# Kernel optimization log

Measured on AMD Instinct MI355X. Metric: run time of the kernel, lower is better.

## Reference

```python
import jax, jax.numpy as jnp
import numpy as np

N = 50000   # nodes
E = 1600000 # edges
G = 512     # graphs in batch
IN_DIM, EMBED, H, D = 64, 128, 4, 32
D1, D2, D3 = 128, 64, 16
NEG_SLOPE = 0.2  # DGL GATConv default


def setup_inputs() -> dict:
    key = jax.random.key(0)
    ks = jax.random.split(key, 16)
    def glorot(k, shape):
        fan = shape[0] + shape[-1]
        return jax.random.normal(k, shape, jnp.float32) * jnp.sqrt(2.0 / fan)
    return {
        "feature": jax.random.normal(ks[0], (N, IN_DIM), jnp.float32),
        "src": jax.random.randint(ks[1], (E,), 0, N, jnp.int32),
        "dst": jax.random.randint(ks[2], (E,), 0, N, jnp.int32),
        "graph_ids": jnp.sort(jax.random.randint(ks[3], (N,), 0, G, jnp.int32)),
        "W0": glorot(ks[4], (IN_DIM, EMBED)), "b0": jnp.zeros((EMBED,), jnp.float32),
        "Wfc": glorot(ks[5], (EMBED, H * D)),
        "attn_l": glorot(ks[6], (H, D)), "attn_r": glorot(ks[7], (H, D)),
        "gat_bias": jnp.zeros((H * D,), jnp.float32),
        "W1": glorot(ks[8], (H * D, D1)), "b1": jnp.zeros((D1,), jnp.float32),
        "W2": glorot(ks[9], (D1, D2)), "b2": jnp.zeros((D2,), jnp.float32),
        "W3": glorot(ks[10], (D2, D3)), "b3": jnp.zeros((D3,), jnp.float32),
    }


def reference(feature, src, dst, graph_ids, W0, b0, Wfc, attn_l, attn_r,
              gat_bias, W1, b1, W2, b2, W3, b3):
    # initial dense embed
    h = feature @ W0 + b0                                   # [N, EMBED]
    # GATConv
    feat = (h @ Wfc).reshape(N, H, D)                       # [N,H,D]
    el = jnp.einsum('nhd,hd->nh', feat, attn_l)             # [N,H]
    er = jnp.einsum('nhd,hd->nh', feat, attn_r)
    e = jax.nn.leaky_relu(el[src] + er[dst], NEG_SLOPE)     # [E,H]
    # segment softmax over incoming edges of each dst node
    m = jax.ops.segment_max(e, dst, num_segments=N)         # [N,H]
    ex = jnp.exp(e - m[dst])                                # [E,H]
    denom = jax.ops.segment_sum(ex, dst, num_segments=N)    # [N,H]
    a = ex / denom[dst]                                     # [E,H]
    msg = a[:, :, None] * feat[src]                         # [E,H,D]
    rst = jax.ops.segment_sum(msg, dst, num_segments=N)     # [N,H,D]
    rst = rst + gat_bias.reshape(1, H, D)
    hn = rst.reshape(N, H * D)
    # AvgPooling per graph
    sums = jax.ops.segment_sum(hn, graph_ids, num_segments=G)           # [G,H*D]
    cnts = jax.ops.segment_sum(jnp.ones((N,), hn.dtype), graph_ids, num_segments=G)
    hg = sums / jnp.maximum(cnts, 1.0)[:, None]
    # dense head
    out = jax.nn.elu(hg)
    out = jax.nn.elu(out @ W1 + b1)
    out = jax.nn.elu(out @ W2 + b2)
    out = out @ W3 + b3                                     # [G, D3]
    atten = a[:, :, None]                                   # [E,H,1] like DGL
    return out, atten
```

## Files before the change

### kernel.cpp

```cpp
#include <hip/hip_runtime.h>
#include <hip/hip_fp16.h>
#include <math.h>

#define N_NODES 50000
#define E_EDGES 1600000
#define G_GRAPHS 512
#define IN_DIM 64
#define EMBED 128
#define HD 128
#define NHEAD 4
#define D1 128
#define D2 64
#define D3 16
#define NEG_SLOPE 0.2f
#define NB ((N_NODES + 127) >> 7)
#define PT_TILE 4096
#define PT_BLOCKS ((E_EDGES + PT_TILE - 1) / PT_TILE)
#define FB_CAP 8192

typedef float vfloat4 __attribute__((ext_vector_type(4)));
typedef float vfloat2 __attribute__((ext_vector_type(2)));
typedef unsigned short ushort_t;

static __device__ __forceinline__ float leaky(float x) { return x > 0.f ? x : NEG_SLOPE * x; }
static __device__ __forceinline__ float compf(float4 v, int i) {
    return i == 0 ? v.x : (i == 1 ? v.y : (i == 2 ? v.z : v.w));
}

__global__ void __launch_bounds__(256) k0hg(const int* __restrict__ dst, int* __restrict__ ghist,
                                            const float* __restrict__ W0, const float* __restrict__ b0,
                                            const float* __restrict__ Wfc, float* __restrict__ Wc,
                                            float* __restrict__ bc) {
    __shared__ int lh[NB];
    const int t = threadIdx.x;
    if (blockIdx.x < PT_BLOCKS) {
        for (int i = t; i < NB; i += 256) lh[i] = 0;
        __syncthreads();
        const long e0 = (long)blockIdx.x * PT_TILE;
#pragma unroll
        for (int k = 0; k < PT_TILE / 256; ++k) {
            long e = e0 + t + k * 256;
            if (e < E_EDGES) atomicAdd(&lh[dst[e] >> 7], 1);
        }
        __syncthreads();
        for (int i = t; i < NB; i += 256) {
            int v = lh[i];
            if (v) atomicAdd(&ghist[i], v);
        }
    } else {
        int tid = (int)(blockIdx.x - PT_BLOCKS) * 256 + t;
        if (tid < IN_DIM * HD) {
            int i = tid >> 7, j = tid & 127;
            float acc = 0.f;
            for (int k = 0; k < EMBED; ++k) acc += W0[i * EMBED + k] * Wfc[k * HD + j];
            Wc[tid] = acc;
        } else if (tid < IN_DIM * HD + HD) {
            int j = tid - IN_DIM * HD;
            float acc = 0.f;
            for (int k = 0; k < EMBED; ++k) acc += b0[k] * Wfc[k * HD + j];
            bc[j] = acc;
        }
    }
}

__global__ void __launch_bounds__(256) k1_gemm(const float* __restrict__ A,
                                               const float* __restrict__ W,
                                               const float* __restrict__ b,
                                               const float* __restrict__ attn_l,
                                               const float* __restrict__ attn_r,
                                               unsigned char* __restrict__ feat,
                                               float* __restrict__ el,
                                               float* __restrict__ er) {
    __shared__ __align__(16) float Ws[IN_DIM * HD];
    __shared__ __align__(16) float As[64][68];
    const int t = threadIdx.x;
    const int cc = t & 31;
    const int rt = t >> 5;
    const int c0 = cc * 4;
    const int r0 = rt * 8;
    const int row0 = blockIdx.x * 64;

    {
        const float4* Wg = (const float4*)W;
        float4* Wl = (float4*)Ws;
#pragma unroll
        for (int j = 0; j < (IN_DIM * HD / 4) / 256; ++j) Wl[t + j * 256] = Wg[t + j * 256];
    }
#pragma unroll
    for (int j = 0; j < 4; ++j) {
        int i2 = t + j * 256;
        int row = i2 >> 4, kq = i2 & 15;
        int gr = row0 + row;
        float4 v = (gr < N_NODES) ? *(const float4*)(A + (size_t)gr * IN_DIM + kq * 4)
                                  : make_float4(0.f, 0.f, 0.f, 0.f);
        *(float4*)&As[row][kq * 4] = v;
    }
    __syncthreads();

    float acc[8][4];
#pragma unroll
    for (int i = 0; i < 8; ++i)
#pragma unroll
        for (int j = 0; j < 4; ++j) acc[i][j] = 0.f;

    for (int k4 = 0; k4 < IN_DIM / 4; ++k4) {
        vfloat4 w0 = *(const vfloat4*)&Ws[(k4 * 4 + 0) * HD + c0];
        vfloat4 w1 = *(const vfloat4*)&Ws[(k4 * 4 + 1) * HD + c0];
        vfloat4 w2 = *(const vfloat4*)&Ws[(k4 * 4 + 2) * HD + c0];
        vfloat4 w3 = *(const vfloat4*)&Ws[(k4 * 4 + 3) * HD + c0];
#pragma unroll
        for (int i = 0; i < 8; ++i) {
            vfloat4 a = *(const vfloat4*)&As[r0 + i][k4 * 4];
#pragma unroll
            for (int j = 0; j < 4; ++j)
                acc[i][j] += a.x * w0[j] + a.y * w1[j] + a.z * w2[j] + a.w * w3[j];
        }
    }

    {
        vfloat4 bcv = *(const vfloat4*)(b + c0);
#pragma unroll
        for (int i = 0; i < 8; ++i)
#pragma unroll
            for (int j = 0; j < 4; ++j) acc[i][j] += bcv[j];
    }

#pragma unroll
    for (int i = 0; i < 8; ++i) {
        int gr = row0 + r0 + i;
        if (gr < N_NODES) {
            unsigned int ww = __builtin_amdgcn_cvt_pk_fp8_f32(acc[i][0], acc[i][1], 0, false);
            ww = __builtin_amdgcn_cvt_pk_fp8_f32(acc[i][2], acc[i][3], ww, true);
            *(unsigned int*)(feat + (size_t)gr * HD + c0) = ww;
        }
    }

    {
        vfloat4 al = *(const vfloat4*)(attn_l + c0);
        vfloat4 ar = *(const vfloat4*)(attn_r + c0);
        float pl[8], pr[8];
#pragma unroll
        for (int i = 0; i < 8; ++i) {
            pl[i] = acc[i][0] * al[0] + acc[i][1] * al[1] + acc[i][2] * al[2] + acc[i][3] * al[3];
            pr[i] = acc[i][0] * ar[0] + acc[i][1] * ar[1] + acc[i][2] * ar[2] + acc[i][3] * ar[3];
        }
#pragma unroll
        for (int off = 1; off <= 4; off <<= 1) {
#pragma unroll
            for (int i = 0; i < 8; ++i) {
                pl[i] += __shfl_xor(pl[i], off);
                pr[i] += __shfl_xor(pr[i], off);
            }
        }
        if ((cc & 7) == 0) {
            const int h = cc >> 3;
#pragma unroll
            for (int i = 0; i < 8; ++i) {
                int gr = row0 + r0 + i;
                if (gr < N_NODES) {
                    el[gr * 4 + h] = pl[i];
                    er[gr * 4 + h] = pr[i];
                }
            }
        }
    }
}

__global__ void __launch_bounds__(64) sc_scan(const int* __restrict__ ghist,
                                              int* __restrict__ coarse_start,
                                              int* __restrict__ cursorp) {
    const int lane = threadIdx.x;
    int run = 0;
    for (int c = 0; c < (NB + 63) / 64; ++c) {
        int i = c * 64 + lane;
        int v = (i < NB) ? ghist[i] : 0;
        int incl = v;
#pragma unroll
        for (int off = 1; off < 64; off <<= 1) {
            int o = __shfl_up(incl, off, 64);
            if (lane >= off) incl += o;
        }
        if (i < NB) {
            coarse_start[i] = run + incl - v;
            cursorp[i] = run + incl - v;
        }
        run += __shfl(incl, 63, 64);
    }
    if (lane == 0) coarse_start[NB] = E_EDGES;
}

__global__ void __launch_bounds__(256) pt_partition(const int* __restrict__ src,
                                                    const int* __restrict__ dst,
                                                    int* __restrict__ cursorp,
                                                    unsigned int* __restrict__ part) {
    __shared__ int hist[4][NB];
    __shared__ int tot[NB], offs[NB], base_s[NB];
    __shared__ int lcur[4][NB];
    __shared__ unsigned int stage[PT_TILE];
    const int t = threadIdx.x, lane = t & 63, wid = t >> 6;
    const long e0 = (long)blockIdx.x * PT_TILE;
    const int cnt = (int)min((long)PT_TILE, (long)E_EDGES - e0);
    for (int i = t; i < NB; i += 256) {
        hist[0][i] = 0; hist[1][i] = 0; hist[2][i] = 0; hist[3][i] = 0;
    }
    __syncthreads();
    unsigned int v[PT_TILE / 256];
#pragma unroll
    for (int k = 0; k < PT_TILE / 256; ++k) {
        int i = t + k * 256;
        if (i < cnt) {
            int d = dst[e0 + i];
            v[k] = ((unsigned int)d << 16) | (unsigned int)src[e0 + i];
            atomicAdd(&hist[wid][d >> 7], 1);
        } else v[k] = 0xFFFFFFFFu;
    }
    __syncthreads();
    for (int i = t; i < NB; i += 256) {
        int h0 = hist[0][i], h1 = hist[1][i], h2 = hist[2][i], h3 = hist[3][i];
        hist[0][i] = 0; hist[1][i] = h0; hist[2][i] = h0 + h1; hist[3][i] = h0 + h1 + h2;
        tot[i] = h0 + h1 + h2 + h3;
    }
    __syncthreads();
    if (wid == 0) {
        int run = 0;
        for (int c = 0; c < (NB + 63) / 64; ++c) {
            int i = c * 64 + lane;
            int vv = (i < NB) ? tot[i] : 0;
            int incl = vv;
#pragma unroll
            for (int off = 1; off < 64; off <<= 1) {
                int o = __shfl_up(incl, off, 64);
                if (lane >= off) incl += o;
            }
            if (i < NB) offs[i] = run + incl - vv;
            run += __shfl(incl, 63, 64);
        }
    }
    __syncthreads();
    for (int i = t; i < NB; i += 256) {
        int tt = tot[i];
        base_s[i] = tt ? atomicAdd(&cursorp[i], tt) : 0;
        int ob = offs[i];
        lcur[0][i] = ob + hist[0][i];
        lcur[1][i] = ob + hist[1][i];
        lcur[2][i] = ob + hist[2][i];
        lcur[3][i] = ob + hist[3][i];
    }
    __syncthreads();
#pragma unroll
    for (int k = 0; k < PT_TILE / 256; ++k) {
        if (v[k] != 0xFFFFFFFFu) {
            int b = v[k] >> 23;
            int pos = atomicAdd(&lcur[wid][b], 1);
            stage[pos] = v[k];
        }
    }
    __syncthreads();
    for (int i = t; i < cnt; i += 256) {
        unsigned int p = stage[i];
        int b = p >> 23;
        part[base_s[b] + (i - offs[b])] = p & 0x7FFFFFu;
    }
}

__global__ void __launch_bounds__(256) fb_fill(const unsigned int* __restrict__ part,
                                               const int* __restrict__ coarse_start,
                                               int* __restrict__ rowstart,
                                               ushort_t* __restrict__ csr_src) {
    const int b = blockIdx.x, t = threadIdx.x, lane = t & 63, wid = t >> 6;
    const int s0 = coarse_start[b], s1 = coarse_start[b + 1];
    const int cnt = s1 - s0;
    __shared__ int degl[4][128], totl[128], offl[128], curl[4][128];
    __shared__ ushort_t lsrc[FB_CAP];
    if (t < 128) { degl[0][t] = 0; degl[1][t] = 0; degl[2][t] = 0; degl[3][t] = 0; }
    __syncthreads();
    for (int i = t; i < cnt; i += 256) {
        unsigned int p = part[s0 + i];
        atomicAdd(&degl[wid][p >> 16], 1);
    }
    __syncthreads();
    if (t < 128) {
        int d0 = degl[0][t], d1 = degl[1][t], d2 = degl[2][t], d3 = degl[3][t];
        degl[0][t] = 0; degl[1][t] = d0; degl[2][t] = d0 + d1; degl[3][t] = d0 + d1 + d2;
        totl[t] = d0 + d1 + d2 + d3;
    }
    __syncthreads();
    if (wid == 0) {
        int run = 0;
        for (int c = 0; c < 2; ++c) {
            int i = c * 64 + lane;
            int vv = totl[i];
            int incl = vv;
#pragma unroll
            for (int off = 1; off < 64; off <<= 1) {
                int o = __shfl_up(incl, off, 64);
                if (lane >= off) incl += o;
            }
            offl[i] = run + incl - vv;
            run += __shfl(incl, 63, 64);
        }
    }
    __syncthreads();
    if (t < 128) {
        int ob = offl[t];
        curl[0][t] = ob + degl[0][t];
        curl[1][t] = ob + degl[1][t];
        curl[2][t] = ob + degl[2][t];
        curl[3][t] = ob + degl[3][t];
        int node = (b << 7) + t;
        if (node < N_NODES) rowstart[node] = s0 + ob;
    }
    if (b == 0 && t == 0) rowstart[N_NODES] = E_EDGES;
    __syncthreads();
    if (cnt <= FB_CAP) {
        for (int i = t; i < cnt; i += 256) {
            unsigned int p = part[s0 + i];
            int pos = atomicAdd(&curl[wid][p >> 16], 1);
            lsrc[pos] = (ushort_t)(p & 0xFFFFu);
        }
        __syncthreads();
        for (int i = t; i < cnt; i += 256) csr_src[s0 + i] = lsrc[i];
    } else {
        for (int i = t; i < cnt; i += 256) {
            unsigned int p = part[s0 + i];
            int pos = atomicAdd(&curl[wid][p >> 16], 1);
            csr_src[s0 + pos] = (ushort_t)(p & 0xFFFFu);
        }
    }
}

__global__ void __launch_bounds__(256) k6_aggregate(
    const ushort_t* __restrict__ csr_src, const int* __restrict__ rowstart,
    const float* __restrict__ el, const float* __restrict__ er,
    const unsigned char* __restrict__ feat, const float* __restrict__ gat_bias,
    float* __restrict__ er_rd, float* __restrict__ hn) {
    __shared__ float s_av[4][64][4];
    __shared__ int s_src[4][64];
    const int wid = threadIdx.x >> 6;
    const int lane = threadIdx.x & 63;
    const int n = blockIdx.x * 4 + wid;
    if (n >= N_NODES) return;
    const int start = rowstart[n];
    const int end = rowstart[n + 1];
    const int deg = end - start;
    const float4 er4 = *(const float4*)(er + n * 4);

    int esrc = 0;
    float4 ex = make_float4(0.f, 0.f, 0.f, 0.f);
    const bool valid = lane < deg;
    if (valid) {
        esrc = csr_src[start + lane];
        const float4 elv = *(const float4*)(el + esrc * 4);
        ex.x = __expf(leaky(elv.x + er4.x));
        ex.y = __expf(leaky(elv.y + er4.y));
        ex.z = __expf(leaky(elv.z + er4.z));
        ex.w = __expf(leaky(elv.w + er4.w));
    }
    float4 sm = ex;
    for (int e = start + lane + 64; e < end; e += 64) {
        int s = csr_src[e];
        const float4 elv = *(const float4*)(el + s * 4);
        sm.x += __expf(leaky(elv.x + er4.x));
        sm.y += __expf(leaky(elv.y + er4.y));
        sm.z += __expf(leaky(elv.z + er4.z));
        sm.w += __expf(leaky(elv.w + er4.w));
    }
#pragma unroll
    for (int off = 32; off; off >>= 1) {
        sm.x += __shfl_xor(sm.x, off);
        sm.y += __shfl_xor(sm.y, off);
        sm.z += __shfl_xor(sm.z, off);
        sm.w += __shfl_xor(sm.w, off);
    }
    float4 rd;
    rd.x = sm.x > 0.f ? 1.f / sm.x : 0.f;
    rd.y = sm.y > 0.f ? 1.f / sm.y : 0.f;
    rd.z = sm.z > 0.f ? 1.f / sm.z : 0.f;
    rd.w = sm.w > 0.f ? 1.f / sm.w : 0.f;
    if (lane == 0) {
        *(float4*)(er_rd + (size_t)n * 8) = er4;
        *(float4*)(er_rd + (size_t)n * 8 + 4) = rd;
    }
    vfloat4 av4;
    av4.x = ex.x * rd.x;
    av4.y = ex.y * rd.y;
    av4.z = ex.z * rd.z;
    av4.w = ex.w * rd.w;
    s_src[wid][lane] = valid ? esrc : 0;
    *(vfloat4*)(&s_av[wid][lane][0]) = av4;

    const int g4 = lane >> 4, gl = lane & 15;
    const int h = gl >> 2;
    float4 a0 = make_float4(0.f, 0.f, 0.f, 0.f);
    float4 a1 = make_float4(0.f, 0.f, 0.f, 0.f);

    if (deg <= 64) {
        const int iters = (deg + 3) >> 2;
        int idx = g4;
        for (int it = 0; it < iters; ++it, idx += 4) {
            const float av = s_av[wid][idx][h];
            const unsigned int cs = (unsigned int)s_src[wid][idx];
            const uint2 w = *(const uint2*)(feat + (size_t)cs * HD + gl * 8);
            const vfloat2 p0 = __builtin_amdgcn_cvt_pk_f32_fp8(w.x, false);
            const vfloat2 p1 = __builtin_amdgcn_cvt_pk_f32_fp8(w.x, true);
            const vfloat2 p2 = __builtin_amdgcn_cvt_pk_f32_fp8(w.y, false);
            const vfloat2 p3 = __builtin_amdgcn_cvt_pk_f32_fp8(w.y, true);
            a0.x += av * p0.x; a0.y += av * p0.y;
            a0.z += av * p1.x; a0.w += av * p1.y;
            a1.x += av * p2.x; a1.y += av * p2.y;
            a1.z += av * p3.x; a1.w += av * p3.y;
        }
    } else {
        const float rh = compf(rd, h);
        const float erh = compf(er4, h);
        for (int e = start + g4; e < end; e += 4) {
            const unsigned int s = csr_src[e];
            const float av = __expf(leaky(el[s * 4 + h] + erh)) * rh;
            const uint2 w = *(const uint2*)(feat + (size_t)s * HD + gl * 8);
            const vfloat2 p0 = __builtin_amdgcn_cvt_pk_f32_fp8(w.x, false);
            const vfloat2 p1 = __builtin_amdgcn_cvt_pk_f32_fp8(w.x, true);
            const vfloat2 p2 = __builtin_amdgcn_cvt_pk_f32_fp8(w.y, false);
            const vfloat2 p3 = __builtin_amdgcn_cvt_pk_f32_fp8(w.y, true);
            a0.x += av * p0.x; a0.y += av * p0.y;
            a0.z += av * p1.x; a0.w += av * p1.y;
            a1.x += av * p2.x; a1.y += av * p2.y;
            a1.z += av * p3.x; a1.w += av * p3.y;
        }
    }
#pragma unroll
    for (int off = 16; off <= 32; off <<= 1) {
        a0.x += __shfl_xor(a0.x, off);
        a0.y += __shfl_xor(a0.y, off);
        a0.z += __shfl_xor(a0.z, off);
        a0.w += __shfl_xor(a0.w, off);
        a1.x += __shfl_xor(a1.x, off);
        a1.y += __shfl_xor(a1.y, off);
        a1.z += __shfl_xor(a1.z, off);
        a1.w += __shfl_xor(a1.w, off);
    }
    if (lane < 16) {
        const float4 b0 = ((const float4*)gat_bias)[gl * 2];
        const float4 b1 = ((const float4*)gat_bias)[gl * 2 + 1];
        float4* hp = (float4*)(hn + (size_t)n * HD + gl * 8);
        hp[0] = make_float4(a0.x + b0.x, a0.y + b0.y, a0.z + b0.z, a0.w + b0.w);
        hp[1] = make_float4(a1.x + b1.x, a1.y + b1.y, a1.z + b1.z, a1.w + b1.w);
    }
}

__global__ void __launch_bounds__(256) k6b_attn(
    const int* __restrict__ src, const int* __restrict__ dst,
    const float* __restrict__ el, const float* __restrict__ er_rd,
    float* __restrict__ a_out) {
    int e = blockIdx.x * 256 + threadIdx.x;
    if (e >= E_EDGES) return;
    const int s = src[e], d = dst[e];
    const float4 el4 = *(const float4*)(el + s * 4);
    const float4 er4 = *(const float4*)(er_rd + (size_t)d * 8);
    const float4 r4 = *(const float4*)(er_rd + (size_t)d * 8 + 4);
    vfloat4 a;
    a.x = __expf(leaky(el4.x + er4.x)) * r4.x;
    a.y = __expf(leaky(el4.y + er4.y)) * r4.y;
    a.z = __expf(leaky(el4.z + er4.z)) * r4.z;
    a.w = __expf(leaky(el4.w + er4.w)) * r4.w;
    __builtin_nontemporal_store(a, (vfloat4*)a_out + e);
}

__global__ void __launch_bounds__(512) k7_pool_mlp(
    const float* __restrict__ hn, const int* __restrict__ graph_ids,
    const float* __restrict__ W1, const float* __restrict__ b1,
    const float* __restrict__ W2, const float* __restrict__ b2,
    const float* __restrict__ W3, const float* __restrict__ b3,
    float* __restrict__ out) {
    const int g = blockIdx.x, t = threadIdx.x;
    const int tt = t & 127, part = t >> 7;
    __shared__ int bounds[2];
    __shared__ double pool[4][128];
    __shared__ double x[128], y[128];
    if (t < 2) {
        const int target = g + t;
        int lo = 0, hi = N_NODES;
        while (lo < hi) {
            int mid = (lo + hi) >> 1;
            if (graph_ids[mid] < target) lo = mid + 1; else hi = mid;
        }
        bounds[t] = lo;
    }
    __syncthreads();
    const int lo = bounds[0], hi = bounds[1];
    double s = 0.0;
    for (int n = lo + part; n < hi; n += 4) s += (double)hn[(size_t)n * HD + tt];
    pool[part][tt] = s;
    __syncthreads();
    if (t < 128) {
        const double cnt = (double)(hi - lo);
        const double sum = pool[0][t] + pool[1][t] + pool[2][t] + pool[3][t];
        const double v = sum / fmax(cnt, 1.0);
        x[t] = v > 0.0 ? v : expm1(v);
    }
    __syncthreads();
    if (t < 128) {
        double acc = (double)b1[t];
        for (int k = 0; k < HD; ++k) acc += x[k] * (double)W1[k * D1 + t];
        y[t] = acc > 0.0 ? acc : expm1(acc);
    }
    __syncthreads();
    if (t < D2) {
        double a2 = (double)b2[t];
        for (int k = 0; k < D1; ++k) a2 += y[k] * (double)W2[k * D2 + t];
        x[t] = a2 > 0.0 ? a2 : expm1(a2);
    }
    __syncthreads();
    if (t < D3) {
        double a3 = (double)b3[t];
        for (int k = 0; k < D2; ++k) a3 += x[k] * (double)W3[k * D3 + t];
        out[g * D3 + t] = (float)a3;
    }
}

extern "C" void kernel_launch(void* const* d_in, const int* in_sizes, int n_in,
                              void* d_out, int out_size, void* d_ws, size_t ws_size,
                              hipStream_t stream) {
    const float* feature = (const float*)d_in[0];
    const int* src = (const int*)d_in[1];
    const int* dst = (const int*)d_in[2];
    const int* graph_ids = (const int*)d_in[3];
    const float* W0 = (const float*)d_in[4];
    const float* b0 = (const float*)d_in[5];
    const float* Wfc = (const float*)d_in[6];
    const float* attn_l = (const float*)d_in[7];
    const float* attn_r = (const float*)d_in[8];
    const float* gat_bias = (const float*)d_in[9];
    const float* W1 = (const float*)d_in[10];
    const float* b1 = (const float*)d_in[11];
    const float* W2 = (const float*)d_in[12];
    const float* b2 = (const float*)d_in[13];
    const float* W3 = (const float*)d_in[14];
    const float* b3 = (const float*)d_in[15];

    char* ws = (char*)d_ws;
    size_t off = 0;
    auto carve = [&](size_t bytes) -> void* {
        void* p = ws + off;
        off += (bytes + 255) & ~(size_t)255;
        return p;
    };
    int* ghist = (int*)carve((size_t)NB * 4);
    const size_t zero_span = off;
    int* coarse_start = (int*)carve((size_t)(NB + 1) * 4);
    int* cursorp = (int*)carve((size_t)NB * 4);
    float* Wc = (float*)carve((size_t)IN_DIM * HD * 4);
    float* bc = (float*)carve((size_t)HD * 4);
    unsigned char* feat = (unsigned char*)carve((size_t)N_NODES * HD);
    float* el = (float*)carve((size_t)N_NODES * 4 * 4);
    float* er = (float*)carve((size_t)N_NODES * 4 * 4);
    float* er_rd = (float*)carve((size_t)N_NODES * 8 * 4);
    int* rowstart = (int*)carve((size_t)(N_NODES + 1) * 4);
    unsigned int* part = (unsigned int*)carve((size_t)E_EDGES * 4);
    ushort_t* csr_src = (ushort_t*)carve((size_t)E_EDGES * 2);

    float* out = (float*)d_out;
    float* hn = out + G_GRAPHS * D3;
    float* a_out = hn;

    (void)hipMemsetAsync(d_ws, 0, zero_span, stream);
    k0hg<<<PT_BLOCKS + 33, 256, 0, stream>>>(dst, ghist, W0, b0, Wfc, Wc, bc);
    k1_gemm<<<(N_NODES + 63) / 64, 256, 0, stream>>>(feature, Wc, bc, attn_l, attn_r,
                                                     feat, el, er);
    sc_scan<<<1, 64, 0, stream>>>(ghist, coarse_start, cursorp);
    pt_partition<<<PT_BLOCKS, 256, 0, stream>>>(src, dst, cursorp, part);
    fb_fill<<<NB, 256, 0, stream>>>(part, coarse_start, rowstart, csr_src);
    k6_aggregate<<<(N_NODES + 3) / 4, 256, 0, stream>>>(csr_src, rowstart, el, er, feat,
                                                        gat_bias, er_rd, hn);
    k7_pool_mlp<<<G_GRAPHS, 512, 0, stream>>>(hn, graph_ids, W1, b1, W2, b2, W3, b3, out);
    k6b_attn<<<(E_EDGES + 255) / 256, 256, 0, stream>>>(src, dst, el, er_rd, a_out);
}
```

Before: 243.7 us.

## Restructure GAT aggregation: lane-per-(edge,head) softmax, packed LDS, deferred normalization

The aggregation kernel now gives each lane one (edge, head) pair in the softmax pass and stores the pre-shifted source offset together with the unnormalized exp in a single packed uint2 LDS entry. Normalization by the reciprocal sum is moved out of the per-edge loop and applied once to the accumulators. The gather loop is unrolled by two edges and uses packed float2 FMAs, aiming to raise memory-level parallelism and cut per-edge ALU and LDS work. The trade-off is a 16-edge stride in the softmax pass, which may need more iterations for higher-degree nodes.

```diff
diff --git a/kernel.cpp b/kernel.cpp
--- a/kernel.cpp
+++ b/kernel.cpp
@@ -23,9 +23,6 @@
 typedef unsigned short ushort_t;
 
 static __device__ __forceinline__ float leaky(float x) { return x > 0.f ? x : NEG_SLOPE * x; }
-static __device__ __forceinline__ float compf(float4 v, int i) {
-    return i == 0 ? v.x : (i == 1 ? v.y : (i == 2 ? v.z : v.w));
-}
 
 __global__ void __launch_bounds__(256) k0hg(const int* __restrict__ dst, int* __restrict__ ghist,
                                             const float* __restrict__ W0, const float* __restrict__ b0,
@@ -334,8 +331,7 @@
     const float* __restrict__ el, const float* __restrict__ er,
     const unsigned char* __restrict__ feat, const float* __restrict__ gat_bias,
     float* __restrict__ er_rd, float* __restrict__ hn) {
-    __shared__ float s_av[4][64][4];
-    __shared__ int s_src[4][64];
+    __shared__ uint2 s_pk[4][64][4];
     const int wid = threadIdx.x >> 6;
     const int lane = threadIdx.x & 63;
     const int n = blockIdx.x * 4 + wid;
@@ -343,107 +339,101 @@
     const int start = rowstart[n];
     const int end = rowstart[n + 1];
     const int deg = end - start;
-    const float4 er4 = *(const float4*)(er + n * 4);
-
-    int esrc = 0;
-    float4 ex = make_float4(0.f, 0.f, 0.f, 0.f);
-    const bool valid = lane < deg;
-    if (valid) {
-        esrc = csr_src[start + lane];
-        const float4 elv = *(const float4*)(el + esrc * 4);
-        ex.x = __expf(leaky(elv.x + er4.x));
-        ex.y = __expf(leaky(elv.y + er4.y));
-        ex.z = __expf(leaky(elv.z + er4.z));
-        ex.w = __expf(leaky(elv.w + er4.w));
-    }
-    float4 sm = ex;
-    for (int e = start + lane + 64; e < end; e += 64) {
-        int s = csr_src[e];
-        const float4 elv = *(const float4*)(el + s * 4);
-        sm.x += __expf(leaky(elv.x + er4.x));
-        sm.y += __expf(leaky(elv.y + er4.y));
-        sm.z += __expf(leaky(elv.z + er4.z));
-        sm.w += __expf(leaky(elv.w + er4.w));
-    }
-#pragma unroll
-    for (int off = 32; off; off >>= 1) {
-        sm.x += __shfl_xor(sm.x, off);
-        sm.y += __shfl_xor(sm.y, off);
-        sm.z += __shfl_xor(sm.z, off);
-        sm.w += __shfl_xor(sm.w, off);
-    }
-    float4 rd;
-    rd.x = sm.x > 0.f ? 1.f / sm.x : 0.f;
-    rd.y = sm.y > 0.f ? 1.f / sm.y : 0.f;
-    rd.z = sm.z > 0.f ? 1.f / sm.z : 0.f;
-    rd.w = sm.w > 0.f ? 1.f / sm.w : 0.f;
-    if (lane == 0) {
-        *(float4*)(er_rd + (size_t)n * 8) = er4;
-        *(float4*)(er_rd + (size_t)n * 8 + 4) = rd;
-    }
-    vfloat4 av4;
-    av4.x = ex.x * rd.x;
-    av4.y = ex.y * rd.y;
-    av4.z = ex.z * rd.z;
-    av4.w = ex.w * rd.w;
-    s_src[wid][lane] = valid ? esrc : 0;
-    *(vfloat4*)(&s_av[wid][lane][0]) = av4;
+
+    const int e0 = lane >> 2;
+    const int h = lane & 3;
+    const float erh = er[n * 4 + h];
+    float sm = 0.f;
+    for (int base = 0; base < deg; base += 16) {
+        const int e = base + e0;
+        const bool v = e < deg;
+        if (v) {
+            const int s = csr_src[start + e];
+            const float ex = __expf(leaky(el[s * 4 + h] + erh));
+            sm += ex;
+            if (e < 64)
+                s_pk[wid][e][h] = make_uint2((unsigned int)s << 7, __float_as_uint(ex));
+        }
+    }
+#pragma unroll
+    for (int off = 4; off <= 32; off <<= 1) sm += __shfl_xor(sm, off);
+    const float rd = sm > 0.f ? 1.f / sm : 0.f;
+    if (lane < 4) {
+        er_rd[(size_t)n * 8 + lane] = erh;
+        er_rd[(size_t)n * 8 + 4 + lane] = rd;
+    }
 
     const int g4 = lane >> 4, gl = lane & 15;
-    const int h = gl >> 2;
-    float4 a0 = make_float4(0.f, 0.f, 0.f, 0.f);
-    float4 a1 = make_float4(0.f, 0.f, 0.f, 0.f);
+    const int h2 = gl >> 2;
+    const float rdh = __shfl(rd, h2);
+    vfloat2 acc0 = {0.f, 0.f}, acc1 = {0.f, 0.f}, acc2 = {0.f, 0.f}, acc3 = {0.f, 0.f};
 
     if (deg <= 64) {
-        const int iters = (deg + 3) >> 2;
+        const uint2* pk = &s_pk[wid][0][h2];
+        const unsigned char* fg = feat + (gl << 3);
         int idx = g4;
-        for (int it = 0; it < iters; ++it, idx += 4) {
-            const float av = s_av[wid][idx][h];
-            const unsigned int cs = (unsigned int)s_src[wid][idx];
-            const uint2 w = *(const uint2*)(feat + (size_t)cs * HD + gl * 8);
-            const vfloat2 p0 = __builtin_amdgcn_cvt_pk_f32_fp8(w.x, false);
-            const vfloat2 p1 = __builtin_amdgcn_cvt_pk_f32_fp8(w.x, true);
-            const vfloat2 p2 = __builtin_amdgcn_cvt_pk_f32_fp8(w.y, false);
-            const vfloat2 p3 = __builtin_amdgcn_cvt_pk_f32_fp8(w.y, true);
-            a0.x += av * p0.x; a0.y += av * p0.y;
-            a0.z += av * p1.x; a0.w += av * p1.y;
-            a1.x += av * p2.x; a1.y += av * p2.y;
-            a1.z += av * p3.x; a1.w += av * p3.y;
+        for (; idx + 4 < deg; idx += 8) {
+            const uint2 pA = pk[idx * 4];
+            const uint2 pB = pk[(idx + 4) * 4];
+            const uint2 wA = *(const uint2*)(fg + pA.x);
+            const uint2 wB = *(const uint2*)(fg + pB.x);
+            const float exA = __uint_as_float(pA.y);
+            const float exB = __uint_as_float(pB.y);
+            const vfloat2 eA = {exA, exA}, eB = {exB, exB};
+            acc0 += eA * __builtin_amdgcn_cvt_pk_f32_fp8(wA.x, false);
+            acc1 += eA * __builtin_amdgcn_cvt_pk_f32_fp8(wA.x, true);
+            acc2 += eA * __builtin_amdgcn_cvt_pk_f32_fp8(wA.y, false);
+            acc3 += eA * __builtin_amdgcn_cvt_pk_f32_fp8(wA.y, true);
+            acc0 += eB * __builtin_amdgcn_cvt_pk_f32_fp8(wB.x, false);
+            acc1 += eB * __builtin_amdgcn_cvt_pk_f32_fp8(wB.x, true);
+            acc2 += eB * __builtin_amdgcn_cvt_pk_f32_fp8(wB.y, false);
+            acc3 += eB * __builtin_amdgcn_cvt_pk_f32_fp8(wB.y, true);
+        }
+        if (idx < deg) {
+            const uint2 p = pk[idx * 4];
+            const uint2 w = *(const uint2*)(fg + p.x);
+            const float ex = __uint_as_float(p.y);
+            const vfloat2 ev = {ex, ex};
+            acc0 += ev * __builtin_amdgcn_cvt_pk_f32_fp8(w.x, false);
+            acc1 += ev * __builtin_amdgcn_cvt_pk_f32_fp8(w.x, true);
+            acc2 += ev * __builtin_amdgcn_cvt_pk_f32_fp8(w.y, false);
+            acc3 += ev * __builtin_amdgcn_cvt_pk_f32_fp8(w.y, true);
         }
     } else {
-        const float rh = compf(rd, h);
-        const float erh = compf(er4, h);
+        const float erh2 = __shfl(erh, h2);
+        const unsigned char* fg = feat + (gl << 3);
         for (int e = start + g4; e < end; e += 4) {
             const unsigned int s = csr_src[e];
-            const float av = __expf(leaky(el[s * 4 + h] + erh)) * rh;
-            const uint2 w = *(const uint2*)(feat + (size_t)s * HD + gl * 8);
-            const vfloat2 p0 = __builtin_amdgcn_cvt_pk_f32_fp8(w.x, false);
-            const vfloat2 p1 = __builtin_amdgcn_cvt_pk_f32_fp8(w.x, true);
-            const vfloat2 p2 = __builtin_amdgcn_cvt_pk_f32_fp8(w.y, false);
-            const vfloat2 p3 = __builtin_amdgcn_cvt_pk_f32_fp8(w.y, true);
-            a0.x += av * p0.x; a0.y += av * p0.y;
-            a0.z += av * p1.x; a0.w += av * p1.y;
-            a1.x += av * p2.x; a1.y += av * p2.y;
-            a1.z += av * p3.x; a1.w += av * p3.y;
-        }
+            const float ex = __expf(leaky(el[s * 4 + h2] + erh2));
+            const vfloat2 ev = {ex, ex};
+            const uint2 w = *(const uint2*)(fg + ((size_t)s << 7));
+            acc0 += ev * __builtin_amdgcn_cvt_pk_f32_fp8(w.x, false);
+            acc1 += ev * __builtin_amdgcn_cvt_pk_f32_fp8(w.x, true);
+            acc2 += ev * __builtin_amdgcn_cvt_pk_f32_fp8(w.y, false);
+            acc3 += ev * __builtin_amdgcn_cvt_pk_f32_fp8(w.y, true);
+        }
+    }
+    {
+        const vfloat2 rv = {rdh, rdh};
+        acc0 *= rv; acc1 *= rv; acc2 *= rv; acc3 *= rv;
     }
 #pragma unroll
     for (int off = 16; off <= 32; off <<= 1) {
-        a0.x += __shfl_xor(a0.x, off);
-        a0.y += __shfl_xor(a0.y, off);
-        a0.z += __shfl_xor(a0.z, off);
-        a0.w += __shfl_xor(a0.w, off);
-        a1.x += __shfl_xor(a1.x, off);
-        a1.y += __shfl_xor(a1.y, off);
-        a1.z += __shfl_xor(a1.z, off);
-        a1.w += __shfl_xor(a1.w, off);
+        acc0.x += __shfl_xor(acc0.x, off);
+        acc0.y += __shfl_xor(acc0.y, off);
+        acc1.x += __shfl_xor(acc1.x, off);
+        acc1.y += __shfl_xor(acc1.y, off);
+        acc2.x += __shfl_xor(acc2.x, off);
+        acc2.y += __shfl_xor(acc2.y, off);
+        acc3.x += __shfl_xor(acc3.x, off);
+        acc3.y += __shfl_xor(acc3.y, off);
     }
     if (lane < 16) {
         const float4 b0 = ((const float4*)gat_bias)[gl * 2];
         const float4 b1 = ((const float4*)gat_bias)[gl * 2 + 1];
         float4* hp = (float4*)(hn + (size_t)n * HD + gl * 8);
-        hp[0] = make_float4(a0.x + b0.x, a0.y + b0.y, a0.z + b0.z, a0.w + b0.w);
-        hp[1] = make_float4(a1.x + b1.x, a1.y + b1.y, a1.z + b1.z, a1.w + b1.w);
+        hp[0] = make_float4(acc0.x + b0.x, acc0.y + b0.y, acc1.x + b0.z, acc1.y + b0.w);
+        hp[1] = make_float4(acc2.x + b1.x, acc2.y + b1.y, acc3.x + b1.z, acc3.y + b1.w);
     }
 }
 
```

After: 250.4 us. 2.8% more time.
